# Kernel tuning notes

Hardware: AMD Instinct MI355X
Metric: run time of the kernel (lower is better)

The kernel has to match this reference:

```python
import jax, jax.numpy as jnp
import numpy as np

ATOM_DIM = 34
GAT_DIM = 128
HID_DIM = 256
G_LAYERS = 3
ALPHA = 0.2
NEG_INF = -9e15  # matches torch zero_vec constant


def setup_inputs() -> dict:
    key = jax.random.key(0)
    ks = jax.random.split(key, 10)
    B, N = 64, 512
    compound = jax.random.normal(ks[0], (B, N, ATOM_DIM), dtype=jnp.float32)
    adj = jax.random.randint(ks[1], (B, N, N), 0, 2, dtype=jnp.int32)
    # xavier_uniform gain=1.414 approx: bound = gain*sqrt(6/(fan_in+fan_out))
    def xavier(k, shape, gain=1.414):
        bound = gain * np.sqrt(6.0 / (shape[-2] + shape[-1]))
        return jax.random.uniform(k, shape, jnp.float32, -bound, bound)
    W_stack = xavier(ks[2], (G_LAYERS, ATOM_DIM, GAT_DIM))        # per-layer W
    a_stack = xavier(ks[3], (G_LAYERS, 2 * GAT_DIM, 1))            # per-layer a
    W_out = xavier(ks[4], (G_LAYERS * GAT_DIM, GAT_DIM))           # gat_out.W
    a_out = xavier(ks[5], (2 * GAT_DIM, 1))                        # gat_out.a
    lim = 1.0 / np.sqrt(GAT_DIM)
    Wc = jax.random.uniform(ks[6], (GAT_DIM, HID_DIM), jnp.float32, -lim, lim)  # W_comp weight (in,out)
    bc = jax.random.uniform(ks[7], (HID_DIM,), jnp.float32, -lim, lim)
    return {"compound": compound, "adj": adj, "W_stack": W_stack,
            "a_stack": a_stack, "W_out": W_out, "a_out": a_out,
            "Wc": Wc, "bc": bc}


def _gat_layer(h, adj, W, a, concat):
    # h: [B,N,Fin], adj: [B,N,N], W: [Fin,Fout], a: [2*Fout,1]
    Wh = jnp.einsum('bnf,fg->bng', h, W)                 # [B,N,Fout]
    Fout = W.shape[1]
    # e[b,i,j] = leakyrelu(Wh_i . a1 + Wh_j . a2) == leakyrelu(cat(Wh_i,Wh_j) @ a)
    src = Wh @ a[:Fout, 0]                               # [B,N]
    dst = Wh @ a[Fout:, 0]                               # [B,N]
    e = jax.nn.leaky_relu(src[:, :, None] + dst[:, None, :], ALPHA)  # [B,N,N]
    scores = jnp.where(adj > 0, e, NEG_INF)
    attention = jax.nn.softmax(scores, axis=2)
    h_prime = jnp.einsum('bij,bjf->bif', attention, Wh)  # [B,N,Fout]
    return jax.nn.elu(h_prime) if concat else h_prime


def reference(compound, adj, W_stack, a_stack, W_out, a_out, Wc, bc):
    heads = [_gat_layer(compound, adj, W_stack[l], a_stack[l], concat=True)
             for l in range(G_LAYERS)]
    multi = jnp.concatenate(heads, axis=2)               # [B,N,G_LAYERS*GAT_DIM]
    x = jax.nn.elu(_gat_layer(multi, adj, W_out, a_out, concat=False))
    x = jax.nn.leaky_relu(jnp.einsum('bnf,fh->bnh', x, Wc) + bc, ALPHA)
    return x  # [B,N,HID_DIM]
```

## Files before the change

### kernel.cpp

```cpp
#include <hip/hip_runtime.h>
#include <hip/hip_bf16.h>
#include <math.h>


#define ALPHA 0.2f
#define LOG2E 1.44269504088896f

#if __has_builtin(__builtin_amdgcn_exp2f)
#define EXP2F(x) __builtin_amdgcn_exp2f(x)
#else
extern "C" __device__ float __ocml_exp2_f32(float);
#define EXP2F(x) __ocml_exp2_f32(x)
#endif

typedef __attribute__((ext_vector_type(8))) short s16x8;
typedef __attribute__((ext_vector_type(4))) float f32x4;

__device__ __forceinline__ ushort bf16_rne(float f) {
  union { float f; unsigned u; } v; v.f = f;
  unsigned r = v.u + 0x7FFFu + ((v.u >> 16) & 1u);
  return (ushort)(r >> 16);
}
__device__ __forceinline__ float bf16_tof(ushort h) {
  union { unsigned u; float f; } v; v.u = ((unsigned)h) << 16;
  return v.f;
}
__device__ __forceinline__ void split_store4(
    ushort* __restrict__ ph, ushort* __restrict__ pl,
    float v0, float v1, float v2, float v3) {
  ushort h0 = bf16_rne(v0), h1 = bf16_rne(v1), h2 = bf16_rne(v2), h3 = bf16_rne(v3);
  *(ushort4*)ph = make_ushort4(h0, h1, h2, h3);
  *(ushort4*)pl = make_ushort4(bf16_rne(v0 - bf16_tof(h0)), bf16_rne(v1 - bf16_tof(h1)),
                               bf16_rne(v2 - bf16_tof(h2)), bf16_rne(v3 - bf16_tof(h3)));
}

__device__ __forceinline__ long wht_off(long batch, int c, int j) {
  return batch * 65536 + (long)(c >> 4) * 8192 + (j >> 5) * 512 +
         ((c & 15) << 3) + (((j >> 3) & 3) << 7) + (j & 7);
}

__device__ __forceinline__ long w_frag_off(int c, int j, int Kd) {
  return (long)(c >> 4) * (Kd * 16) + (j >> 5) * 512 +
         ((c & 15) << 3) + (((j >> 3) & 3) << 7) + (j & 7);
}

#define WHT_SLOT 8388608L

__global__ __launch_bounds__(256) void wt_prep(
    const float* __restrict__ W, ushort* __restrict__ TH, ushort* __restrict__ TL,
    const int Kd, const int Nd)
{
  const int idx = blockIdx.x * 256 + threadIdx.x;
  if (idx >= Kd * Nd) return;
  const int k = idx / Nd, n = idx % Nd;
  const float v = W[idx];
  const ushort h = bf16_rne(v);
  const long o = w_frag_off(n, k, Kd);
  TH[o] = h;
  TL[o] = bf16_rne(v - bf16_tof(h));
}

__global__ __launch_bounds__(256) void front_union(
    const float* __restrict__ A, const float* __restrict__ Wst,
    const float* __restrict__ ast,
    ushort* __restrict__ whtBase, float* __restrict__ srcB, float* __restrict__ dstB,
    const int* __restrict__ adj, unsigned* __restrict__ mask,
    const float* __restrict__ W_out, ushort* __restrict__ WoT_H, ushort* __restrict__ WoT_L)
{
  __shared__ float AsT[34][36];
  __shared__ float Ws[34][128];
  const int t = threadIdx.x;
  const int g = blockIdx.x / 83, r83 = blockIdx.x - g * 83;

  if (r83 >= 48) {
    if (r83 < 80) {
      const int mb = g * 32 + (r83 - 48);
      const int gid = mb * 256 + t;
      const int4* __restrict__ p = (const int4*)(adj + (long)gid * 32);
      unsigned m = 0;
#pragma unroll
      for (int k = 0; k < 8; k++) {
        const int4 v = p[k];
        m |= (v.x > 0 ? 1u : 0u) << (4 * k);
        m |= (v.y > 0 ? 1u : 0u) << (4 * k + 1);
        m |= (v.z > 0 ? 1u : 0u) << (4 * k + 2);
        m |= (v.w > 0 ? 1u : 0u) << (4 * k + 3);
      }
      mask[gid] = m;
    } else {
      const int wb = g * 3 + (r83 - 80);
      const int idx = wb * 256 + t;
      const int k = idx / 128, n = idx % 128;
      const float v = W_out[idx];
      const ushort h = bf16_rne(v);
      const long o = w_frag_off(n, k, 384);
      WoT_H[o] = h;
      WoT_L[o] = bf16_rne(v - bf16_tof(h));
    }
    return;
  }

  const int bid = g * 48 + r83;
  const int l = bid >> 10;
  const float* __restrict__ W = Wst + (long)l * 34 * 128;
  const float* __restrict__ avec = ast + (long)l * 256;
  ushort* __restrict__ whtH = whtBase + (long)l * WHT_SLOT;
  ushort* __restrict__ whtL = whtH + 4194304;
  float* __restrict__ src = srcB + (long)l * 32768;
  float* __restrict__ dst = dstB + (long)l * 32768;
  const long row0 = (long)(bid & 1023) * 32;
  const int cg = t & 31, rg = t >> 5;
  {
    const int r = t >> 3, l8 = t & 7;
#pragma unroll
    for (int q = 0; q < 5; q++) {
      int k = l8 + q * 8;
      if (k < 34) AsT[k][r] = A[(row0 + r) * 34 + k];
    }
  }
  {
    int idx = t;
#pragma unroll
    for (int i = 0; i < 17; i++, idx += 256)
      Ws[idx >> 7][idx & 127] = W[idx];
  }
  __syncthreads();

  float acc[4][4];
#pragma unroll
  for (int r = 0; r < 4; r++)
#pragma unroll
    for (int c = 0; c < 4; c++) acc[r][c] = 0.f;
#pragma unroll 2
  for (int k = 0; k < 34; k++) {
    const float4 wv = *(const float4*)&Ws[k][cg * 4];
    const float4 av = *(const float4*)&AsT[k][rg * 4];
#define GFMA(r, a) \
    acc[r][0] += (a) * wv.x; acc[r][1] += (a) * wv.y; \
    acc[r][2] += (a) * wv.z; acc[r][3] += (a) * wv.w;
    GFMA(0, av.x) GFMA(1, av.y) GFMA(2, av.z) GFMA(3, av.w)
#undef GFMA
  }

  {
    const long batch = row0 >> 9;
    const int j = (int)(row0 & 511) + rg * 4;
#pragma unroll
    for (int cc = 0; cc < 4; cc++) {
      const long o = wht_off(batch, cg * 4 + cc, j);
      split_store4(&whtH[o], &whtL[o], acc[0][cc], acc[1][cc], acc[2][cc], acc[3][cc]);
    }
  }

  const float4 a1 = *(const float4*)&avec[cg * 4];
  const float4 a2 = *(const float4*)&avec[128 + cg * 4];
#pragma unroll
  for (int r = 0; r < 4; r++) {
    float s = acc[r][0]*a1.x + acc[r][1]*a1.y + acc[r][2]*a1.z + acc[r][3]*a1.w;
    float d = acc[r][0]*a2.x + acc[r][1]*a2.y + acc[r][2]*a2.z + acc[r][3]*a2.w;
#pragma unroll
    for (int w = 1; w < 32; w <<= 1) {
      s += __shfl_xor(s, w, 64);
      d += __shfl_xor(d, w, 64);
    }
    if (cg == 0) {
      src[row0 + rg * 4 + r] = s * LOG2E;
      dst[row0 + rg * 4 + r] = d * LOG2E;
    }
  }
}


#define LD_SET(S, KB) \
  S##0H = *(const s16x8*)&bH[(KB) * 512]; \
  S##0L = *(const s16x8*)&bL[(KB) * 512]; \
  S##1H = *(const s16x8*)&bH[8192 + (KB) * 512]; \
  S##1L = *(const s16x8*)&bL[8192 + (KB) * 512];

#define MF(a, b, c) c = __builtin_amdgcn_mfma_f32_16x16x32_bf16(a, b, c, 0, 0, 0)

#define STEP(S, KB) { \
  const int k0_ = ((KB) * 32 + q * 8) ^ ((((KB) >> 1) & 7) << 3); \
  const s16x8 a0_ = *(const s16x8*)&As[m16][k0_]; \
  const s16x8 a1_ = *(const s16x8*)&As[16 + m16][k0_]; \
  MF(a0_, S##0H, acc00); MF(a0_, S##1H, acc01); \
  MF(a1_, S##0H, acc10); MF(a1_, S##1H, acc11); \
  MF(a0_, S##0L, acc00); MF(a0_, S##1L, acc01); \
  MF(a1_, S##0L, acc10); MF(a1_, S##1L, acc11); \
  if ((KB) + 4 < 16) { LD_SET(S, (KB) + 4) } }

__global__ __launch_bounds__(256, 4) void fused_attn(
    const unsigned* __restrict__ mask,
    const float* __restrict__ srcB, const float* __restrict__ dstB,
    const ushort* __restrict__ whtBase,
    float* __restrict__ out, const int ostride)
{
  __shared__ ushort As[32][520];
  __shared__ float dstS[544];
  __shared__ float invS[32];
  __shared__ float wredM[4];
  const int t = threadIdx.x;
  const int l = blockIdx.z;
  const float* __restrict__ src = srcB + (long)l * 32768;
  const float* __restrict__ dstv = dstB + (long)l * 32768;
  const ushort* __restrict__ whtH = whtBase + (long)l * WHT_SLOT;
  const ushort* __restrict__ whtL = whtH + 4194304;
  const int ocoff = l * 128;
  const int flat = blockIdx.y * 16 + blockIdx.x;
  const int swz = (flat & 7) * 128 + (flat >> 3);
  const long base = (long)(swz >> 4) * 512;
  const int i0 = (swz & 15) * 32;

  const int wv = t >> 6, lane = t & 63;
  const int m16 = lane & 15, q = lane >> 4;
  const int n0 = wv * 32;
  const ushort* __restrict__ bH = whtH + base * 128 + wv * 16384 + lane * 8;
  const ushort* __restrict__ bL = whtL + base * 128 + wv * 16384 + lane * 8;
  s16x8 sA0H, sA0L, sA1H, sA1L, sB0H, sB0L, sB1H, sB1L;
  s16x8 sC0H, sC0L, sC1H, sC1L, sD0H, sD0L, sD1H, sD1L;
  LD_SET(sA, 0)
  LD_SET(sB, 1)
  LD_SET(sC, 2)
  LD_SET(sD, 3)

  {
    const float d0 = dstv[base + t];
    const float d1 = dstv[base + t + 256];
    dstS[t + (t >> 6) * 4] = d0;
    const int t2 = t + 256;
    dstS[t2 + (t2 >> 6) * 4] = d1;
    float mx = fmaxf(d0, d1);
#pragma unroll
    for (int w = 1; w < 64; w <<= 1) mx = fmaxf(mx, __shfl_xor(mx, w, 64));
    if ((t & 63) == 0) wredM[t >> 6] = mx;
  }
  __syncthreads();
  const float md = fmaxf(fmaxf(wredM[0], wredM[1]), fmaxf(wredM[2], wredM[3]));

  {
    const int r = t >> 3, l8 = t & 7;
    const long i = base + i0 + r;
    const float si = src[i];
    const uint2 mw2 = *(const uint2*)(mask + i * 16 + 2 * l8);
    const float em = si + md;
    const float m = fmaxf(em, ALPHA * em);
    const float* __restrict__ dp = &dstS[l8 * 68];
    const int jb = l8 * 64;
    const int xs = l8 << 3;
    float sum = 0.f;
#pragma unroll
    for (int g = 0; g < 16; g++) {
      const float4 dv = *(const float4*)&dp[g * 4];
      const unsigned w = ((g & 8) ? mw2.y : mw2.x) >> ((g & 7) * 4);
      float e0 = si + dv.x, e1 = si + dv.y, e2 = si + dv.z, e3 = si + dv.w;
      e0 = fmaxf(e0, ALPHA * e0) - m; e1 = fmaxf(e1, ALPHA * e1) - m;
      e2 = fmaxf(e2, ALPHA * e2) - m; e3 = fmaxf(e3, ALPHA * e3) - m;
      float p0 = EXP2F(e0), p1 = EXP2F(e1), p2 = EXP2F(e2), p3 = EXP2F(e3);
      p0 = (w & 1u) ? p0 : 0.f;
      p1 = (w & 2u) ? p1 : 0.f;
      p2 = (w & 4u) ? p2 : 0.f;
      p3 = (w & 8u) ? p3 : 0.f;
      sum += (p0 + p1) + (p2 + p3);
      union { __hip_bfloat162 b; unsigned u; } u01, u23;
      u01.b = __float22bfloat162_rn(make_float2(p0, p1));
      u23.b = __float22bfloat162_rn(make_float2(p2, p3));
      *(uint2*)&As[r][(jb + g * 4) ^ xs] = make_uint2(u01.u, u23.u);
    }
#pragma unroll
    for (int w = 1; w < 8; w <<= 1) sum += __shfl_xor(sum, w, 64);
    if (l8 == 0) invS[r] = 1.f / sum;
  }
  __syncthreads();

  f32x4 acc00 = {0.f,0.f,0.f,0.f}, acc01 = {0.f,0.f,0.f,0.f};
  f32x4 acc10 = {0.f,0.f,0.f,0.f}, acc11 = {0.f,0.f,0.f,0.f};
#pragma unroll
  for (int kp = 0; kp < 4; kp++) {
    STEP(sA, 4 * kp)
    STEP(sB, 4 * kp + 1)
    STEP(sC, 4 * kp + 2)
    STEP(sD, 4 * kp + 3)
  }
#pragma unroll
  for (int reg = 0; reg < 4; reg++) {
    const int row = q * 4 + reg;
    const float li0 = invS[row], li1 = invS[16 + row];
    float v00 = acc00[reg] * li0, v01 = acc01[reg] * li0;
    float v10 = acc10[reg] * li1, v11 = acc11[reg] * li1;
    v00 = v00 > 0.f ? v00 : __expf(v00) - 1.f;
    v01 = v01 > 0.f ? v01 : __expf(v01) - 1.f;
    v10 = v10 > 0.f ? v10 : __expf(v10) - 1.f;
    v11 = v11 > 0.f ? v11 : __expf(v11) - 1.f;
    float* o0 = out + (base + i0 + row) * (long)ostride + ocoff + n0 + m16;
    float* o1 = out + (base + i0 + 16 + row) * (long)ostride + ocoff + n0 + m16;
    o0[0] = v00; o0[16] = v01;
    o1[0] = v10; o1[16] = v11;
  }
}

template<int K, int KC, int MODE>
__global__ __launch_bounds__(256) void mfma_gemm(
    const float* __restrict__ A,
    const ushort* __restrict__ BTH, const ushort* __restrict__ BTL,
    const float* __restrict__ bias, float* __restrict__ outF,
    ushort* __restrict__ whtH, ushort* __restrict__ whtL,
    const float* __restrict__ avec, float* __restrict__ src, float* __restrict__ dst,
    const int ostride)
{
  constexpr int KP = KC + 8;
  __shared__ ushort AsH[32][KP];
  __shared__ ushort AsL[32][KP];
  __shared__ float sredS[4][32], sredD[4][32];
  const int t = threadIdx.x;
  const long row0 = (long)blockIdx.x * 32;
  const int ncoff = (MODE == 1) ? blockIdx.y * 128 : 0;

  const int wv = t >> 6, lane = t & 63;
  const int m16 = lane & 15, q = lane >> 4;
  const int n0 = wv * 32;
  const ushort* __restrict__ bh0 = BTH + (long)((ncoff + n0) >> 4) * (K * 16) + lane * 8;
  const ushort* __restrict__ bl0 = BTL + (long)((ncoff + n0) >> 4) * (K * 16) + lane * 8;

  f32x4 acc[2][2];
#pragma unroll
  for (int m = 0; m < 2; m++)
#pragma unroll
    for (int n = 0; n < 2; n++) acc[m][n] = (f32x4){0.f, 0.f, 0.f, 0.f};

  for (int kc = 0; kc < K; kc += KC) {
    constexpr int NIT = (32 * KC / 4) / 256;
#pragma unroll
    for (int it = 0; it < NIT; it++) {
      const int idx = t + it * 256;
      const int r = idx / (KC / 4), k4 = idx % (KC / 4);
      const float4 v = *(const float4*)&A[(row0 + r) * (long)K + kc + k4 * 4];
      split_store4(&AsH[r][k4 * 4], &AsL[r][k4 * 4], v.x, v.y, v.z, v.w);
    }
    __syncthreads();
#pragma unroll
    for (int ks = 0; ks < KC / 32; ks++) {
      const int k0 = ks * 32 + q * 8;
      const s16x8 a0H = *(const s16x8*)&AsH[m16][k0];
      const s16x8 a0L = *(const s16x8*)&AsL[m16][k0];
      const s16x8 a1H = *(const s16x8*)&AsH[16 + m16][k0];
      const s16x8 a1L = *(const s16x8*)&AsL[16 + m16][k0];
      const int bo = ((kc >> 5) + ks) * 512;
      const s16x8 b0H = *(const s16x8*)&bh0[bo];
      const s16x8 b0L = *(const s16x8*)&bl0[bo];
      const s16x8 b1H = *(const s16x8*)&bh0[K * 16 + bo];
      const s16x8 b1L = *(const s16x8*)&bl0[K * 16 + bo];
      acc[0][0] = __builtin_amdgcn_mfma_f32_16x16x32_bf16(a0H, b0H, acc[0][0], 0, 0, 0);
      acc[0][1] = __builtin_amdgcn_mfma_f32_16x16x32_bf16(a0H, b1H, acc[0][1], 0, 0, 0);
      acc[1][0] = __builtin_amdgcn_mfma_f32_16x16x32_bf16(a1H, b0H, acc[1][0], 0, 0, 0);
      acc[1][1] = __builtin_amdgcn_mfma_f32_16x16x32_bf16(a1H, b1H, acc[1][1], 0, 0, 0);
      acc[0][0] = __builtin_amdgcn_mfma_f32_16x16x32_bf16(a0L, b0H, acc[0][0], 0, 0, 0);
      acc[0][1] = __builtin_amdgcn_mfma_f32_16x16x32_bf16(a0L, b1H, acc[0][1], 0, 0, 0);
      acc[1][0] = __builtin_amdgcn_mfma_f32_16x16x32_bf16(a1L, b0H, acc[1][0], 0, 0, 0);
      acc[1][1] = __builtin_amdgcn_mfma_f32_16x16x32_bf16(a1L, b1H, acc[1][1], 0, 0, 0);
      acc[0][0] = __builtin_amdgcn_mfma_f32_16x16x32_bf16(a0H, b0L, acc[0][0], 0, 0, 0);
      acc[0][1] = __builtin_amdgcn_mfma_f32_16x16x32_bf16(a0H, b1L, acc[0][1], 0, 0, 0);
      acc[1][0] = __builtin_amdgcn_mfma_f32_16x16x32_bf16(a1H, b0L, acc[1][0], 0, 0, 0);
      acc[1][1] = __builtin_amdgcn_mfma_f32_16x16x32_bf16(a1H, b1L, acc[1][1], 0, 0, 0);
    }
    __syncthreads();
  }

  if (MODE == 0) {
    const long batch = row0 >> 9;
    const int iloc = (int)(row0 & 511);
#pragma unroll
    for (int m = 0; m < 2; m++)
#pragma unroll
      for (int n = 0; n < 2; n++) {
        const int c = n0 + n * 16 + m16;
        const int j = iloc + m * 16 + q * 4;
        const long o = wht_off(batch, c, j);
        const f32x4 v = acc[m][n];
        split_store4(&whtH[o], &whtL[o], v[0], v[1], v[2], v[3]);
      }
    const float a10 = avec[n0 + m16], a11 = avec[n0 + 16 + m16];
    const float a20 = avec[128 + n0 + m16], a21 = avec[128 + n0 + 16 + m16];
#pragma unroll
    for (int m = 0; m < 2; m++) {
#pragma unroll
      for (int reg = 0; reg < 4; reg++) {
        float s = acc[m][0][reg] * a10 + acc[m][1][reg] * a11;
        float d = acc[m][0][reg] * a20 + acc[m][1][reg] * a21;
#pragma unroll
        for (int w = 1; w < 16; w <<= 1) {
          s += __shfl_xor(s, w, 64);
          d += __shfl_xor(d, w, 64);
        }
        if (m16 == 0) {
          const int row = m * 16 + q * 4 + reg;
          sredS[wv][row] = s;
          sredD[wv][row] = d;
        }
      }
    }
    __syncthreads();
    if (t < 32) {
      const float s = sredS[0][t] + sredS[1][t] + sredS[2][t] + sredS[3][t];
      const float d = sredD[0][t] + sredD[1][t] + sredD[2][t] + sredD[3][t];
      src[row0 + t] = s * LOG2E;
      dst[row0 + t] = d * LOG2E;
    }
  } else {
#pragma unroll
    for (int m = 0; m < 2; m++)
#pragma unroll
      for (int n = 0; n < 2; n++) {
        const int c = ncoff + n0 + n * 16 + m16;
        const float bv = bias[c];
#pragma unroll
        for (int reg = 0; reg < 4; reg++) {
          float v = acc[m][n][reg] + bv;
          v = fmaxf(v, ALPHA * v);
          outF[(row0 + m * 16 + q * 4 + reg) * (long)ostride + c] = v;
        }
      }
  }
}

extern "C" void kernel_launch(void* const* d_in, const int* in_sizes, int n_in,
                              void* d_out, int out_size, void* d_ws, size_t ws_size,
                              hipStream_t stream) {
  const float* compound = (const float*)d_in[0];
  const int*   adj      = (const int*)d_in[1];
  const float* W_stack  = (const float*)d_in[2];
  const float* a_stack  = (const float*)d_in[3];
  const float* W_out    = (const float*)d_in[4];
  const float* a_out    = (const float*)d_in[5];
  const float* Wc       = (const float*)d_in[6];
  const float* bc       = (const float*)d_in[7];
  float* out = (float*)d_out;

  ushort* wht_all = (ushort*)d_ws;
  float* f     = (float*)d_ws;
  float* multi = f + 12582912;
  float* x     = multi;
  ushort* WcT_H = (ushort*)(multi + 5000000);
  ushort* WcT_L = WcT_H + 32768;

  unsigned* mask = (unsigned*)d_out;
  float* doutF = (float*)d_out;
  float* srcB = doutF + 524288;
  float* dstB = srcB + 4 * 32768;
  ushort* WoT_H = (ushort*)(dstB + 4 * 32768);
  ushort* WoT_L = WoT_H + 98304;
  float* src3 = srcB + 3 * 32768;
  float* dst3 = dstB + 3 * 32768;

  front_union<<<5312, 256, 0, stream>>>(
      compound, W_stack, a_stack, wht_all, srcB, dstB,
      adj, mask, W_out, WoT_H, WoT_L);
  fused_attn<<<dim3(16, 64, 3), 256, 0, stream>>>(
      mask, srcB, dstB, wht_all, multi, 384);
  mfma_gemm<384, 192, 0><<<1024, 256, 0, stream>>>(
      multi, WoT_H, WoT_L, nullptr, nullptr, wht_all, wht_all + 4194304,
      a_out, src3, dst3, 0);
  fused_attn<<<dim3(16, 64, 1), 256, 0, stream>>>(
      mask, src3, dst3, wht_all, x, 128);
  wt_prep<<<128, 256, 0, stream>>>(Wc, WcT_H, WcT_L, 128, 256);
  mfma_gemm<128, 128, 1><<<dim3(1024, 2), 256, 0, stream>>>(
      x, WcT_H, WcT_L, bc, out, nullptr, nullptr, nullptr, nullptr, nullptr, 256);
}
```

Baseline: 230.9 us.

## Fold Wc prep into GEMM launch, register-prefetch B fragments, hoist attn loads

Removes the separate wt_prep launch by adding 128 extra blocks to the first mfma_gemm that split Wc into bf16 hi/lo fragments, and moves WcT storage into a spare workspace slot. The GEMM inner loop now double-buffers B fragments in registers (even/odd sets loaded one step ahead) so global loads overlap MFMAs. In fused_attn, the src and mask loads are issued before the dst reduction barrier to hide their latency. The cost is higher register pressure in the GEMM and a shared launch for unrelated work.

```diff
diff --git a/kernel.cpp b/kernel.cpp
--- a/kernel.cpp
+++ b/kernel.cpp
@@ -15,6 +15,8 @@
 
 typedef __attribute__((ext_vector_type(8))) short s16x8;
 typedef __attribute__((ext_vector_type(4))) float f32x4;
+
+#define MF(a, b, c) c = __builtin_amdgcn_mfma_f32_16x16x32_bf16(a, b, c, 0, 0, 0)
 
 __device__ __forceinline__ ushort bf16_rne(float f) {
   union { float f; unsigned u; } v; v.f = f;
@@ -45,20 +47,6 @@
 }
 
 #define WHT_SLOT 8388608L
-
-__global__ __launch_bounds__(256) void wt_prep(
-    const float* __restrict__ W, ushort* __restrict__ TH, ushort* __restrict__ TL,
-    const int Kd, const int Nd)
-{
-  const int idx = blockIdx.x * 256 + threadIdx.x;
-  if (idx >= Kd * Nd) return;
-  const int k = idx / Nd, n = idx % Nd;
-  const float v = W[idx];
-  const ushort h = bf16_rne(v);
-  const long o = w_frag_off(n, k, Kd);
-  TH[o] = h;
-  TL[o] = bf16_rne(v - bf16_tof(h));
-}
 
 __global__ __launch_bounds__(256) void front_union(
     const float* __restrict__ A, const float* __restrict__ Wst,
@@ -176,8 +164,6 @@
   S##0L = *(const s16x8*)&bL[(KB) * 512]; \
   S##1H = *(const s16x8*)&bH[8192 + (KB) * 512]; \
   S##1L = *(const s16x8*)&bL[8192 + (KB) * 512];
-
-#define MF(a, b, c) c = __builtin_amdgcn_mfma_f32_16x16x32_bf16(a, b, c, 0, 0, 0)
 
 #define STEP(S, KB) { \
   const int k0_ = ((KB) * 32 + q * 8) ^ ((((KB) >> 1) & 7) << 3); \
@@ -222,6 +208,10 @@
   LD_SET(sB, 1)
   LD_SET(sC, 2)
   LD_SET(sD, 3)
+  const int r1 = t >> 3, l8 = t & 7;
+  const long irow = base + i0 + r1;
+  const float si = src[irow];
+  const uint2 mw2 = *(const uint2*)(mask + irow * 16 + 2 * l8);
 
   {
     const float d0 = dstv[base + t];
@@ -238,10 +228,6 @@
   const float md = fmaxf(fmaxf(wredM[0], wredM[1]), fmaxf(wredM[2], wredM[3]));
 
   {
-    const int r = t >> 3, l8 = t & 7;
-    const long i = base + i0 + r;
-    const float si = src[i];
-    const uint2 mw2 = *(const uint2*)(mask + i * 16 + 2 * l8);
     const float em = si + md;
     const float m = fmaxf(em, ALPHA * em);
     const float* __restrict__ dp = &dstS[l8 * 68];
@@ -264,11 +250,11 @@
       union { __hip_bfloat162 b; unsigned u; } u01, u23;
       u01.b = __float22bfloat162_rn(make_float2(p0, p1));
       u23.b = __float22bfloat162_rn(make_float2(p2, p3));
-      *(uint2*)&As[r][(jb + g * 4) ^ xs] = make_uint2(u01.u, u23.u);
+      *(uint2*)&As[r1][(jb + g * 4) ^ xs] = make_uint2(u01.u, u23.u);
     }
 #pragma unroll
     for (int w = 1; w < 8; w <<= 1) sum += __shfl_xor(sum, w, 64);
-    if (l8 == 0) invS[r] = 1.f / sum;
+    if (l8 == 0) invS[r1] = 1.f / sum;
   }
   __syncthreads();
 
@@ -297,6 +283,26 @@
     o1[0] = v10; o1[16] = v11;
   }
 }
+
+
+#define GLD(S, KB) \
+  S##0H = *(const s16x8*)&bh0[(KB) * 512]; \
+  S##0L = *(const s16x8*)&bl0[(KB) * 512]; \
+  S##1H = *(const s16x8*)&bh0[K * 16 + (KB) * 512]; \
+  S##1L = *(const s16x8*)&bl0[K * 16 + (KB) * 512];
+
+#define GSTEP(S, KS) { \
+  const int k0_ = (KS) * 32 + q * 8; \
+  const s16x8 a0H_ = *(const s16x8*)&AsH[m16][k0_]; \
+  const s16x8 a0L_ = *(const s16x8*)&AsL[m16][k0_]; \
+  const s16x8 a1H_ = *(const s16x8*)&AsH[16 + m16][k0_]; \
+  const s16x8 a1L_ = *(const s16x8*)&AsL[16 + m16][k0_]; \
+  MF(a0H_, S##0H, acc[0][0]); MF(a0H_, S##1H, acc[0][1]); \
+  MF(a1H_, S##0H, acc[1][0]); MF(a1H_, S##1H, acc[1][1]); \
+  MF(a0L_, S##0H, acc[0][0]); MF(a0L_, S##1H, acc[0][1]); \
+  MF(a1L_, S##0H, acc[1][0]); MF(a1L_, S##1H, acc[1][1]); \
+  MF(a0H_, S##0L, acc[0][0]); MF(a0H_, S##1L, acc[0][1]); \
+  MF(a1H_, S##0L, acc[1][0]); MF(a1H_, S##1L, acc[1][1]); }
 
 template<int K, int KC, int MODE>
 __global__ __launch_bounds__(256) void mfma_gemm(
@@ -312,6 +318,19 @@
   __shared__ ushort AsL[32][KP];
   __shared__ float sredS[4][32], sredD[4][32];
   const int t = threadIdx.x;
+
+  if (MODE == 0 && blockIdx.x >= 1024) {
+    const int idx = ((int)blockIdx.x - 1024) * 256 + t;
+    const int k = idx >> 8, n = idx & 255;
+    const float v = bias[idx];
+    const ushort h = bf16_rne(v);
+    const long o = w_frag_off(n, k, 128);
+    ushort* __restrict__ WcTH = (ushort*)outF;
+    WcTH[o] = h;
+    WcTH[32768 + o] = bf16_rne(v - bf16_tof(h));
+    return;
+  }
+
   const long row0 = (long)blockIdx.x * 32;
   const int ncoff = (MODE == 1) ? blockIdx.y * 128 : 0;
 
@@ -321,12 +340,17 @@
   const ushort* __restrict__ bh0 = BTH + (long)((ncoff + n0) >> 4) * (K * 16) + lane * 8;
   const ushort* __restrict__ bl0 = BTL + (long)((ncoff + n0) >> 4) * (K * 16) + lane * 8;
 
+  s16x8 gE0H, gE0L, gE1H, gE1L, gO0H, gO0L, gO1H, gO1L;
+  GLD(gE, 0)
+  GLD(gO, 1)
+
   f32x4 acc[2][2];
 #pragma unroll
   for (int m = 0; m < 2; m++)
 #pragma unroll
     for (int n = 0; n < 2; n++) acc[m][n] = (f32x4){0.f, 0.f, 0.f, 0.f};
 
+#pragma unroll
   for (int kc = 0; kc < K; kc += KC) {
     constexpr int NIT = (32 * KC / 4) / 256;
 #pragma unroll
@@ -338,29 +362,12 @@
     }
     __syncthreads();
 #pragma unroll
-    for (int ks = 0; ks < KC / 32; ks++) {
-      const int k0 = ks * 32 + q * 8;
-      const s16x8 a0H = *(const s16x8*)&AsH[m16][k0];
-      const s16x8 a0L = *(const s16x8*)&AsL[m16][k0];
-      const s16x8 a1H = *(const s16x8*)&AsH[16 + m16][k0];
-      const s16x8 a1L = *(const s16x8*)&AsL[16 + m16][k0];
-      const int bo = ((kc >> 5) + ks) * 512;
-      const s16x8 b0H = *(const s16x8*)&bh0[bo];
-      const s16x8 b0L = *(const s16x8*)&bl0[bo];
-      const s16x8 b1H = *(const s16x8*)&bh0[K * 16 + bo];
-      const s16x8 b1L = *(const s16x8*)&bl0[K * 16 + bo];
-      acc[0][0] = __builtin_amdgcn_mfma_f32_16x16x32_bf16(a0H, b0H, acc[0][0], 0, 0, 0);
-      acc[0][1] = __builtin_amdgcn_mfma_f32_16x16x32_bf16(a0H, b1H, acc[0][1], 0, 0, 0);
-      acc[1][0] = __builtin_amdgcn_mfma_f32_16x16x32_bf16(a1H, b0H, acc[1][0], 0, 0, 0);
-      acc[1][1] = __builtin_amdgcn_mfma_f32_16x16x32_bf16(a1H, b1H, acc[1][1], 0, 0, 0);
-      acc[0][0] = __builtin_amdgcn_mfma_f32_16x16x32_bf16(a0L, b0H, acc[0][0], 0, 0, 0);
-      acc[0][1] = __builtin_amdgcn_mfma_f32_16x16x32_bf16(a0L, b1H, acc[0][1], 0, 0, 0);
-      acc[1][0] = __builtin_amdgcn_mfma_f32_16x16x32_bf16(a1L, b0H, acc[1][0], 0, 0, 0);
-      acc[1][1] = __builtin_amdgcn_mfma_f32_16x16x32_bf16(a1L, b1H, acc[1][1], 0, 0, 0);
-      acc[0][0] = __builtin_amdgcn_mfma_f32_16x16x32_bf16(a0H, b0L, acc[0][0], 0, 0, 0);
-      acc[0][1] = __builtin_amdgcn_mfma_f32_16x16x32_bf16(a0H, b1L, acc[0][1], 0, 0, 0);
-      acc[1][0] = __builtin_amdgcn_mfma_f32_16x16x32_bf16(a1H, b0L, acc[1][0], 0, 0, 0);
-      acc[1][1] = __builtin_amdgcn_mfma_f32_16x16x32_bf16(a1H, b1L, acc[1][1], 0, 0, 0);
+    for (int ks2 = 0; ks2 < KC / 64; ks2++) {
+      const int kbE = (kc >> 5) + 2 * ks2;
+      GSTEP(gE, 2 * ks2)
+      if (kbE + 2 < K / 32) { GLD(gE, kbE + 2) }
+      GSTEP(gO, 2 * ks2 + 1)
+      if (kbE + 3 < K / 32) { GLD(gO, kbE + 3) }
     }
     __syncthreads();
   }
@@ -439,7 +446,7 @@
   float* f     = (float*)d_ws;
   float* multi = f + 12582912;
   float* x     = multi;
-  ushort* WcT_H = (ushort*)(multi + 5000000);
+  ushort* WcT_H = wht_all + WHT_SLOT;
   ushort* WcT_L = WcT_H + 32768;
 
   unsigned* mask = (unsigned*)d_out;
@@ -456,12 +463,11 @@
       adj, mask, W_out, WoT_H, WoT_L);
   fused_attn<<<dim3(16, 64, 3), 256, 0, stream>>>(
       mask, srcB, dstB, wht_all, multi, 384);
-  mfma_gemm<384, 192, 0><<<1024, 256, 0, stream>>>(
-      multi, WoT_H, WoT_L, nullptr, nullptr, wht_all, wht_all + 4194304,
+  mfma_gemm<384, 192, 0><<<1152, 256, 0, stream>>>(
+      multi, WoT_H, WoT_L, Wc, (float*)WcT_H, wht_all, wht_all + 4194304,
       a_out, src3, dst3, 0);
   fused_attn<<<dim3(16, 64, 1), 256, 0, stream>>>(
       mask, src3, dst3, wht_all, x, 128);
-  wt_prep<<<128, 256, 0, stream>>>(Wc, WcT_H, WcT_L, 128, 256);
   mfma_gemm<128, 128, 1><<<dim3(1024, 2), 256, 0, stream>>>(
       x, WcT_H, WcT_L, bc, out, nullptr, nullptr, nullptr, nullptr, nullptr, 256);
 }
```

Result: no change. 234.9 us (+1.7%).
